# Performance work log

Measured on AMD Instinct MI355X. Metric: run time of the kernel, lower is better.

## Reference

```python
import jax, jax.numpy as jnp
import numpy as np

B, T, C, K, NH, HID, L, NC = 16, 500, 512, 7, 8, 2048, 3, 2
HD = C // NH
SCALE = float(1.0 / np.sqrt(HD))


def setup_inputs() -> dict:
    key = jax.random.key(0)
    ks = jax.random.split(key, 24)
    rn = lambda k, sh, s=0.02: jax.random.normal(k, sh, jnp.float32) * s
    return {
        'x': jax.random.normal(ks[0], (B, T, C), jnp.float32),
        'dw_w': rn(ks[1], (L, NC, C, 1, K)),   # depthwise conv kernels (groups=C)
        'dw_b': rn(ks[2], (L, NC, C)),
        'pw_w': rn(ks[3], (L, NC, C, C)),       # pointwise 1x1 conv weights [out,in]
        'pw_b': rn(ks[4], (L, NC, C)),
        'cln_g': jnp.ones((L, NC, C), jnp.float32),
        'cln_b': jnp.zeros((L, NC, C), jnp.float32),
        'wq': rn(ks[5], (L, C, C)), 'bq': rn(ks[6], (L, C)),
        'wk': rn(ks[7], (L, C, C)), 'bk': rn(ks[8], (L, C)),
        'wv': rn(ks[9], (L, C, C)), 'bv': rn(ks[10], (L, C)),
        'wo': rn(ks[11], (L, C, C)), 'bo': rn(ks[12], (L, C)),
        'aln_g': jnp.ones((L, C), jnp.float32), 'aln_b': jnp.zeros((L, C), jnp.float32),
        'w1': rn(ks[13], (L, HID, C)), 'b1': rn(ks[14], (L, HID)),
        'w2': rn(ks[15], (L, C, HID)), 'b2': rn(ks[16], (L, C)),
        'fln_g': jnp.ones((L, C), jnp.float32), 'fln_b': jnp.zeros((L, C), jnp.float32),
    }


def _ln(x, g, b):
    m = x.mean(-1, keepdims=True)
    v = ((x - m) ** 2).mean(-1, keepdims=True)
    return (x - m) / jnp.sqrt(v + 1e-5) * g + b


def _conv_block(x, w, b, pw, pb, g, be):
    # x: (B, C, T). Depthwise conv (groups=C), padding K//2 keeps T.
    out = jax.lax.conv_general_dilated(
        x, w, window_strides=(1,), padding=[(K // 2, K // 2)],
        feature_group_count=C, dimension_numbers=('NCH', 'OIH', 'NCH')) + b[None, :, None]
    out = jnp.einsum('bct,oc->bot', out, pw) + pb[None, :, None]  # pointwise 1x1
    out = _ln(out.transpose(0, 2, 1), g, be).transpose(0, 2, 1)
    return out


def _attn(x, wq, bq, wk, bk, wv, bv, wo, bo):
    Bx, Tx, Cx = x.shape
    def split(h):
        return h.reshape(Bx, Tx, NH, HD).transpose(0, 2, 1, 3)  # (B,H,T,HD)
    q = split(x @ wq.T + bq)
    k = split(x @ wk.T + bk)
    v = split(x @ wv.T + bv)
    att = jnp.einsum('bhqd,bhkd->bhqk', q, k) * SCALE
    mask = jnp.tril(jnp.ones((Tx, Tx), bool))
    att = jnp.where(mask, att, -1e10)
    att = jax.nn.softmax(att, axis=-1)
    y = jnp.einsum('bhqk,bhkd->bhqd', att, v)
    y = y.transpose(0, 2, 1, 3).reshape(Bx, Tx, Cx)
    return y @ wo.T + bo


def _block(x, l, dw_w, dw_b, pw_w, pw_b, cln_g, cln_b, wq, bq, wk, bk, wv, bv,
           wo, bo, aln_g, aln_b, w1, b1, w2, b2, fln_g, fln_b):
    out = x.transpose(0, 2, 1)  # (B, C, T)
    for c in range(NC):
        out = _conv_block(out, dw_w[l, c], dw_b[l, c], pw_w[l, c], pw_b[l, c],
                          cln_g[l, c], cln_b[l, c])
    out = out.transpose(0, 2, 1)  # (B, T, C)
    out = _attn(out, wq[l], bq[l], wk[l], bk[l], wv[l], bv[l], wo[l], bo[l])
    out = _ln(out, aln_g[l], aln_b[l])
    out = _ln(jax.nn.relu(out @ w1[l].T + b1[l]) @ w2[l].T + b2[l], fln_g[l], fln_b[l])
    return out  # eval mode: dropouts are identity


def reference(x, dw_w, dw_b, pw_w, pw_b, cln_g, cln_b, wq, bq, wk, bk, wv, bv,
              wo, bo, aln_g, aln_b, w1, b1, w2, b2, fln_g, fln_b):
    outs = []
    h = x
    for l in range(L):
        h = _block(h, l, dw_w, dw_b, pw_w, pw_b, cln_g, cln_b, wq, bq, wk, bk,
                   wv, bv, wo, bo, aln_g, aln_b, w1, b1, w2, b2, fln_g, fln_b)
        outs.append(h)
    return tuple(outs)
```

## Files before the change

### kernel.cpp

```cpp
#include <hip/hip_runtime.h>
#include <hip/hip_bf16.h>

namespace {
constexpr int B = 16, T = 500, C = 512, KW = 7, NH = 8, HD = 64, HID = 2048;
constexpr int M = B * T;
constexpr float SCALE = 0.125f;
constexpr int BTC = B * T * C;
constexpr int CC = C * C;
constexpr int SEG_PW0 = 0;
constexpr int SEG_PW1 = CC;
constexpr int SEG_WQ  = 2 * CC;
constexpr int SEG_WK  = 3 * CC;
constexpr int SEG_WV  = 4 * CC;
constexpr int SEG_WO  = 5 * CC;
constexpr int SEG_W1  = 6 * CC;
constexpr int SEG_W2  = 6 * CC + HID * C;
constexpr int SEG_END = 6 * CC + 2 * HID * C;
}

typedef short s16x8 __attribute__((ext_vector_type(8)));
typedef float f32x4v __attribute__((ext_vector_type(4)));
typedef unsigned short u16x4 __attribute__((ext_vector_type(4)));

__device__ __forceinline__ unsigned int bfrne(float f) {
  unsigned int u = __float_as_uint(f);
  return (u + 0x7fffu + ((u >> 16) & 1u)) >> 16;
}
__device__ __forceinline__ unsigned int pack2(float a, float b) {
  return bfrne(a) | (bfrne(b) << 16);
}

__device__ __forceinline__ void gl_lds16(const unsigned short* g,
                                         unsigned short* l) {
  __builtin_amdgcn_global_load_lds(
      (const __attribute__((address_space(1))) void*)g,
      (__attribute__((address_space(3))) void*)l, 16, 0, 0);
}

__global__ __launch_bounds__(256) void cvtw_kernel(
    const float* __restrict__ pw0, const float* __restrict__ pw1,
    const float* __restrict__ wqp, const float* __restrict__ wkp,
    const float* __restrict__ wvp, const float* __restrict__ wop,
    const float* __restrict__ w1p, const float* __restrict__ w2p,
    unsigned short* __restrict__ dst) {
  size_t e = ((size_t)blockIdx.x * 256 + threadIdx.x) * 8;
  const float* src;
  size_t off;
  if      (e < SEG_PW1) { src = pw0; off = e - SEG_PW0; }
  else if (e < SEG_WQ)  { src = pw1; off = e - SEG_PW1; }
  else if (e < SEG_WK)  { src = wqp; off = e - SEG_WQ; }
  else if (e < SEG_WV)  { src = wkp; off = e - SEG_WK; }
  else if (e < SEG_WO)  { src = wvp; off = e - SEG_WV; }
  else if (e < SEG_W1)  { src = wop; off = e - SEG_WO; }
  else if (e < SEG_W2)  { src = w1p; off = e - SEG_W1; }
  else                  { src = w2p; off = e - SEG_W2; }
  float4 a = *(const float4*)(src + off);
  float4 b = *(const float4*)(src + off + 4);
  uint4 o;
  o.x = pack2(a.x, a.y); o.y = pack2(a.z, a.w);
  o.z = pack2(b.x, b.y); o.w = pack2(b.z, b.w);
  *(uint4*)(dst + e) = o;
}

__global__ __launch_bounds__(256) void biascat_kernel(
    const float* __restrict__ bq, const float* __restrict__ bk,
    const float* __restrict__ bv, float* __restrict__ dst) {
  int i = blockIdx.x * 256 + threadIdx.x;
  float v = (i < 512) ? bq[i] : (i < 1024 ? bk[i - 512] : bv[i - 1024]);
  dst[i] = v;
}

template <bool RELU, bool YBF, bool SPLIT>
__global__ __launch_bounds__(512) void gemm_mfma(
    const unsigned short* __restrict__ Xb,
    const unsigned short* __restrict__ Wb, const float* __restrict__ bias,
    void* __restrict__ Yv, int N, int K) {
  __shared__ unsigned short As[3][128 * 32];
  __shared__ unsigned short Bs[3][128 * 32];
  const int tid = threadIdx.x;
  const int w = tid >> 6, lane = tid & 63;
  const int quad = lane >> 4, r15 = lane & 15;

  const int ks = SPLIT ? blockIdx.z : 0;
  const int K2 = SPLIT ? (K >> 1) : K;
  const int kbase = ks * K2;

  const int gx = gridDim.x;
  const int nwg = gx * gridDim.y;
  const int orig = blockIdx.y * gx + blockIdx.x;
  const int q8 = nwg >> 3, r8 = nwg & 7;
  const int xcd = orig & 7, sidx = orig >> 3;
  const int tile =
      (xcd < r8 ? xcd * (q8 + 1) : r8 * (q8 + 1) + (xcd - r8) * q8) + sidx;
  const int n0 = (tile % gx) * 128;
  const int m0 = (tile / gx) * 128;

  const int srow = lane >> 2;
  const int gch = ((lane & 3) ^ ((lane >> 3) & 3)) * 8;
  const size_t xsrc =
      (size_t)min(m0 + w * 16 + srow, M - 1) * K + kbase + gch;
  const size_t wsrc = (size_t)(n0 + w * 16 + srow) * K + kbase + gch;

  auto issue = [&](int buf, int k0) {
    gl_lds16(Xb + xsrc + k0, &As[buf][w * 512]);
    gl_lds16(Wb + wsrc + k0, &Bs[buf][w * 512]);
  };

  const int wm = w >> 1, wn = w & 1;
  const int mh = wm * 32, nh = wn * 64;
  const int c0 = (quad ^ ((r15 >> 1) & 3)) * 8;

  f32x4v acc[2][4];
#pragma unroll
  for (int i = 0; i < 2; ++i)
#pragma unroll
    for (int j = 0; j < 4; ++j) acc[i][j] = {0.f, 0.f, 0.f, 0.f};

  const int nk = K2 / 32;
  issue(0, 0);
  issue(1, 32);
  int cur = 0, nxt = 2;
  for (int c = 0; c < nk; ++c) {
    if (c + 1 < nk)
      asm volatile("s_waitcnt vmcnt(2)" ::: "memory");
    else
      asm volatile("s_waitcnt vmcnt(0)" ::: "memory");
    __builtin_amdgcn_s_barrier();
    __builtin_amdgcn_sched_barrier(0);
    if (c + 2 < nk) issue(nxt, (c + 2) * 32);
    const unsigned short* Ac = As[cur];
    const unsigned short* Bc = Bs[cur];
    s16x8 af[2], bg[4];
#pragma unroll
    for (int im = 0; im < 2; ++im)
      af[im] = *(const s16x8*)&Ac[(mh + im * 16 + r15) * 32 + c0];
#pragma unroll
    for (int in = 0; in < 4; ++in)
      bg[in] = *(const s16x8*)&Bc[(nh + in * 16 + r15) * 32 + c0];
#pragma unroll
    for (int in = 0; in < 4; ++in)
#pragma unroll
      for (int im = 0; im < 2; ++im)
        acc[im][in] = __builtin_amdgcn_mfma_f32_16x16x32_bf16(
            af[im], bg[in], acc[im][in], 0, 0, 0);
    cur = (cur == 2) ? 0 : cur + 1;
    nxt = (nxt == 2) ? 0 : nxt + 1;
  }
  float* Yf = (float*)Yv + (SPLIT ? (size_t)ks * M * N : 0);
#pragma unroll
  for (int in = 0; in < 4; ++in) {
    int col = n0 + nh + in * 16 + r15;
    float bv = bias[col];
    if (SPLIT && ks) bv = 0.f;
#pragma unroll
    for (int im = 0; im < 2; ++im) {
      int rowb = m0 + mh + im * 16 + quad * 4;
#pragma unroll
      for (int r = 0; r < 4; ++r) {
        int row = rowb + r;
        if (row < M) {
          float v = acc[im][in][r] + bv;
          if (RELU) v = fmaxf(v, 0.f);
          if (YBF)
            ((unsigned short*)Yv)[(size_t)row * N + col] =
                (unsigned short)bfrne(v);
          else
            Yf[(size_t)row * N + col] = v;
        }
      }
    }
  }
}

__global__ __launch_bounds__(256) void dwconv_kernel(
    const float* __restrict__ X, const float* __restrict__ W,
    const float* __restrict__ bias, unsigned short* __restrict__ Y) {
  int gid = blockIdx.x * 256 + threadIdx.x;
  int b = blockIdx.y;
  int e = gid * 2;
  int t = e >> 9;
  int c = e & 511;
  float acc0 = bias[c], acc1 = bias[c + 1];
  size_t base = (size_t)b * T * C;
#pragma unroll
  for (int k = 0; k < KW; ++k) {
    int tt = t + k - 3;
    if (tt >= 0 && tt < T) {
      float2 xv = *(const float2*)&X[base + (size_t)tt * C + c];
      acc0 += xv.x * W[c * KW + k];
      acc1 += xv.y * W[(c + 1) * KW + k];
    }
  }
  *(unsigned int*)&Y[base + e] = pack2(acc0, acc1);
}

template <bool DUAL, bool SUM2>
__global__ __launch_bounds__(256) void ln_kernel(
    const float* __restrict__ X, const float* __restrict__ g,
    const float* __restrict__ bta, float* __restrict__ Y,
    unsigned short* __restrict__ Yb) {
  int row = blockIdx.x * 4 + (threadIdx.x >> 6);
  int lane = threadIdx.x & 63;
  const float* x = X + (size_t)row * C + lane * 8;
  float4 a = *(const float4*)x;
  float4 b2 = *(const float4*)(x + 4);
  float v[8] = {a.x, a.y, a.z, a.w, b2.x, b2.y, b2.z, b2.w};
  if (SUM2) {
    const float* x2 = x + (size_t)BTC;
    float4 a2 = *(const float4*)x2;
    float4 b3 = *(const float4*)(x2 + 4);
    v[0] += a2.x; v[1] += a2.y; v[2] += a2.z; v[3] += a2.w;
    v[4] += b3.x; v[5] += b3.y; v[6] += b3.z; v[7] += b3.w;
  }
  float s = 0.f, ss = 0.f;
#pragma unroll
  for (int i = 0; i < 8; ++i) {
    s += v[i];
    ss += v[i] * v[i];
  }
#pragma unroll
  for (int off = 32; off; off >>= 1) {
    s += __shfl_xor(s, off);
    ss += __shfl_xor(ss, off);
  }
  float mean = s * (1.f / C);
  float var = ss * (1.f / C) - mean * mean;
  var = fmaxf(var, 0.f);
  float rstd = rsqrtf(var + 1e-5f);
  float4 g0 = *(const float4*)(g + lane * 8);
  float4 g1 = *(const float4*)(g + lane * 8 + 4);
  float4 be0 = *(const float4*)(bta + lane * 8);
  float4 be1 = *(const float4*)(bta + lane * 8 + 4);
  float gg[8] = {g0.x, g0.y, g0.z, g0.w, g1.x, g1.y, g1.z, g1.w};
  float bb[8] = {be0.x, be0.y, be0.z, be0.w, be1.x, be1.y, be1.z, be1.w};
  float o[8];
#pragma unroll
  for (int i = 0; i < 8; ++i) o[i] = (v[i] - mean) * rstd * gg[i] + bb[i];
  float* y = Y + (size_t)row * C + lane * 8;
  float4 w0 = {o[0], o[1], o[2], o[3]};
  float4 w1 = {o[4], o[5], o[6], o[7]};
  *(float4*)y = w0;
  *(float4*)(y + 4) = w1;
  if (DUAL) {
    uint4 ob;
    ob.x = pack2(o[0], o[1]); ob.y = pack2(o[2], o[3]);
    ob.z = pack2(o[4], o[5]); ob.w = pack2(o[6], o[7]);
    *(uint4*)(Yb + (size_t)row * C + lane * 8) = ob;
  }
}

__global__ __launch_bounds__(256) void attn_mfma_kernel(
    const unsigned short* __restrict__ QKV, unsigned short* __restrict__ Yb) {
  constexpr int QS = 3 * C;
  constexpr int LDK = 72;
  __shared__ __align__(16) unsigned short Ks[64 * LDK];
  __shared__ __align__(16) unsigned short Vt[64 * LDK];
  __shared__ __align__(16) unsigned short Ps[4][16 * LDK];
  const int tid = threadIdx.x;
  const int lane = tid & 63, w = tid >> 6;
  const int quad = lane >> 4, r15 = lane & 15;
  const int qt = blockIdx.x, hh = blockIdx.y, b = blockIdx.z;
  const int q0 = qt * 64;
  const size_t hbase = (size_t)hh * HD;

  s16x8 qa[2];
  {
    int qr = min(q0 + w * 16 + r15, T - 1);
    const unsigned short* qp = QKV + ((size_t)b * T + qr) * QS + hbase;
#pragma unroll
    for (int ks = 0; ks < 2; ++ks)
      qa[ks] = *(const s16x8*)(qp + ks * 32 + quad * 8);
  }

  f32x4v oacc[4];
  float mm[4], ll[4];
#pragma unroll
  for (int i = 0; i < 4; ++i) {
    oacc[i] = {0.f, 0.f, 0.f, 0.f};
    mm[i] = -1e30f;
    ll[i] = 0.f;
  }

  const int krow = tid >> 2, kd = (tid & 3) * 16;
  const int vk4 = (tid >> 4) * 4, vd4 = (tid & 15) * 4;

  const int kend = min(q0 + 63, T - 1);
  for (int key0 = 0; key0 <= kend; key0 += 64) {
    __syncthreads();
    {
      int key = key0 + krow;
      if (key < T) {
        const unsigned short* kp =
            QKV + ((size_t)b * T + key) * QS + C + hbase + kd;
        uint4 k0 = *(const uint4*)kp;
        uint4 k1 = *(const uint4*)(kp + 8);
        *(uint4*)&Ks[krow * LDK + kd] = k0;
        *(uint4*)&Ks[krow * LDK + kd + 8] = k1;
      } else {
        uint4 z = {0u, 0u, 0u, 0u};
        *(uint4*)&Ks[krow * LDK + kd] = z;
        *(uint4*)&Ks[krow * LDK + kd + 8] = z;
      }
    }
    {
      u16x4 va[4];
#pragma unroll
      for (int j = 0; j < 4; ++j) {
        int key = key0 + vk4 + j;
        if (key < T) {
          va[j] = *(const u16x4*)(QKV + ((size_t)b * T + key) * QS + 2 * C +
                                  hbase + vd4);
        } else {
          va[j] = (u16x4){0, 0, 0, 0};
        }
      }
#pragma unroll
      for (int i = 0; i < 4; ++i) {
        uint2 o2;
        o2.x = (unsigned int)va[0][i] | ((unsigned int)va[1][i] << 16);
        o2.y = (unsigned int)va[2][i] | ((unsigned int)va[3][i] << 16);
        *(uint2*)&Vt[(vd4 + i) * LDK + vk4] = o2;
      }
    }
    __syncthreads();

    f32x4v sa[4];
#pragma unroll
    for (int nt = 0; nt < 4; ++nt) {
      s16x8 kb0 = *(const s16x8*)&Ks[(nt * 16 + r15) * LDK + quad * 8];
      s16x8 kb1 = *(const s16x8*)&Ks[(nt * 16 + r15) * LDK + 32 + quad * 8];
      f32x4v z = {0.f, 0.f, 0.f, 0.f};
      z = __builtin_amdgcn_mfma_f32_16x16x32_bf16(qa[0], kb0, z, 0, 0, 0);
      z = __builtin_amdgcn_mfma_f32_16x16x32_bf16(qa[1], kb1, z, 0, 0, 0);
      sa[nt] = z;
    }
    const bool diag = (key0 == q0);

#pragma unroll
    for (int r = 0; r < 4; ++r) {
      int q = q0 + w * 16 + quad * 4 + r;
      float sv[4];
#pragma unroll
      for (int nt = 0; nt < 4; ++nt) {
        sv[nt] = sa[nt][r] * SCALE;
        if (diag && (key0 + nt * 16 + r15 > q)) sv[nt] = -1e30f;
      }
      float mx = fmaxf(fmaxf(sv[0], sv[1]), fmaxf(sv[2], sv[3]));
      mx = fmaxf(mx, __shfl_xor(mx, 8));
      mx = fmaxf(mx, __shfl_xor(mx, 4));
      mx = fmaxf(mx, __shfl_xor(mx, 2));
      mx = fmaxf(mx, __shfl_xor(mx, 1));
      float mnew = fmaxf(mm[r], mx);
      float alpha = __expf(mm[r] - mnew);
      float ps = 0.f;
#pragma unroll
      for (int nt = 0; nt < 4; ++nt) {
        float p = __expf(sv[nt] - mnew);
        ps += p;
        Ps[w][(quad * 4 + r) * LDK + nt * 16 + r15] =
            (unsigned short)bfrne(p);
      }
      ps += __shfl_xor(ps, 8);
      ps += __shfl_xor(ps, 4);
      ps += __shfl_xor(ps, 2);
      ps += __shfl_xor(ps, 1);
      ll[r] = ll[r] * alpha + ps;
      mm[r] = mnew;
#pragma unroll
      for (int dt = 0; dt < 4; ++dt) oacc[dt][r] *= alpha;
    }
    asm volatile("s_waitcnt lgkmcnt(0)" ::: "memory");
    __builtin_amdgcn_sched_barrier(0);

    s16x8 pa0 = *(const s16x8*)&Ps[w][r15 * LDK + quad * 8];
    s16x8 pa1 = *(const s16x8*)&Ps[w][r15 * LDK + 32 + quad * 8];
#pragma unroll
    for (int dt = 0; dt < 4; ++dt) {
      s16x8 vb0 = *(const s16x8*)&Vt[(dt * 16 + r15) * LDK + quad * 8];
      s16x8 vb1 = *(const s16x8*)&Vt[(dt * 16 + r15) * LDK + 32 + quad * 8];
      oacc[dt] =
          __builtin_amdgcn_mfma_f32_16x16x32_bf16(pa0, vb0, oacc[dt], 0, 0, 0);
      oacc[dt] =
          __builtin_amdgcn_mfma_f32_16x16x32_bf16(pa1, vb1, oacc[dt], 0, 0, 0);
    }
  }

#pragma unroll
  for (int r = 0; r < 4; ++r) {
    int q = q0 + w * 16 + quad * 4 + r;
    if (q < T) {
      float inv = 1.f / ll[r];
      unsigned short* yp = Yb + ((size_t)b * T + q) * C + hbase;
#pragma unroll
      for (int dt = 0; dt < 4; ++dt)
        yp[dt * 16 + r15] = (unsigned short)bfrne(oacc[dt][r] * inv);
    }
  }
}

extern "C" void kernel_launch(void* const* d_in, const int* in_sizes, int n_in,
                              void* d_out, int out_size, void* d_ws,
                              size_t ws_size, hipStream_t stream) {
  const float* x     = (const float*)d_in[0];
  const float* dw_w  = (const float*)d_in[1];
  const float* dw_b  = (const float*)d_in[2];
  const float* pw_w  = (const float*)d_in[3];
  const float* pw_b  = (const float*)d_in[4];
  const float* cln_g = (const float*)d_in[5];
  const float* cln_b = (const float*)d_in[6];
  const float* wq    = (const float*)d_in[7];
  const float* bq    = (const float*)d_in[8];
  const float* wk    = (const float*)d_in[9];
  const float* bk    = (const float*)d_in[10];
  const float* wv    = (const float*)d_in[11];
  const float* bv    = (const float*)d_in[12];
  const float* wo    = (const float*)d_in[13];
  const float* bo    = (const float*)d_in[14];
  const float* aln_g = (const float*)d_in[15];
  const float* aln_b = (const float*)d_in[16];
  const float* w1    = (const float*)d_in[17];
  const float* b1    = (const float*)d_in[18];
  const float* w2    = (const float*)d_in[19];
  const float* b2    = (const float*)d_in[20];
  const float* fln_g = (const float*)d_in[21];
  const float* fln_b = (const float*)d_in[22];

  float* ws = (float*)d_ws;
  float* A  = ws;
  float* Bf = ws + (size_t)BTC;
  float* R0 = ws + (size_t)2 * BTC;
  float* R1 = ws + (size_t)3 * BTC;
  float* R2 = ws + (size_t)4 * BTC;
  unsigned short* WA = (unsigned short*)(ws + (size_t)5 * BTC);
  float* out = (float*)d_out;

  unsigned short* xbf   = (unsigned short*)Bf;
  unsigned short* qkvbf = (unsigned short*)R0;
  unsigned short* fbf   = (unsigned short*)R2;
  unsigned short* hbf   = (unsigned short*)A;
  float* qkvb = A;

  dim3 blk(256);
  dim3 blkG(512);
  dim3 gemmC2(C / 128, 63, 2);
  dim3 gemmQKV(3 * C / 128, 63);
  dim3 gemmH(HID / 128, 63);
  dim3 convG(T * C / 512, B);
  dim3 attnG((T + 63) / 64, NH, B);
  int cvtwB = SEG_END / 2048;

  for (int l = 0; l < 3; ++l) {
    float* h = out + (size_t)l * BTC;
    const float* hin = (l == 0) ? x : out + (size_t)(l - 1) * BTC;
    cvtw_kernel<<<cvtwB, blk, 0, stream>>>(
        pw_w + (size_t)(2 * l) * CC, pw_w + (size_t)(2 * l + 1) * CC,
        wq + (size_t)l * CC, wk + (size_t)l * CC, wv + (size_t)l * CC,
        wo + (size_t)l * CC, w1 + (size_t)l * HID * C,
        w2 + (size_t)l * C * HID, WA);
    biascat_kernel<<<6, blk, 0, stream>>>(bq + (size_t)l * C,
                                          bk + (size_t)l * C,
                                          bv + (size_t)l * C, qkvb);
    for (int cb = 0; cb < 2; ++cb) {
      int lc = l * 2 + cb;
      const float* src = (cb == 0) ? hin : h;
      dwconv_kernel<<<convG, blk, 0, stream>>>(src, dw_w + (size_t)lc * C * KW,
                                               dw_b + (size_t)lc * C, xbf);
      gemm_mfma<false, false, true><<<gemmC2, blkG, 0, stream>>>(
          xbf, WA + (cb ? SEG_PW1 : SEG_PW0), pw_b + (size_t)lc * C, R0, C, C);
      if (cb == 0)
        ln_kernel<false, true><<<M / 4, blk, 0, stream>>>(
            R0, cln_g + (size_t)lc * C, cln_b + (size_t)lc * C, h, nullptr);
      else
        ln_kernel<true, true><<<M / 4, blk, 0, stream>>>(
            R0, cln_g + (size_t)lc * C, cln_b + (size_t)lc * C, h, xbf);
    }
    gemm_mfma<false, true, false><<<gemmQKV, blkG, 0, stream>>>(
        xbf, WA + SEG_WQ, qkvb, qkvbf, 3 * C, C);
    attn_mfma_kernel<<<attnG, blk, 0, stream>>>(qkvbf, xbf);
    gemm_mfma<false, false, true><<<gemmC2, blkG, 0, stream>>>(
        xbf, WA + SEG_WO, bo + (size_t)l * C, R0, C, C);
    ln_kernel<true, true><<<M / 4, blk, 0, stream>>>(
        R0, aln_g + (size_t)l * C, aln_b + (size_t)l * C, h, fbf);
    gemm_mfma<true, true, false><<<gemmH, blkG, 0, stream>>>(
        fbf, WA + SEG_W1, b1 + (size_t)l * HID, hbf, HID, C);
    gemm_mfma<false, false, true><<<gemmC2, blkG, 0, stream>>>(
        hbf, WA + SEG_W2, b2 + (size_t)l * C, R0, C, HID);
    ln_kernel<false, true><<<M / 4, blk, 0, stream>>>(
        R0, fln_g + (size_t)l * C, fln_b + (size_t)l * C, h, nullptr);
  }
}
```

Before: 977.6 us.

## Restructure causal attention: 128-query blocks, register-prefetched K/V, swizzled V tile

The attention kernel now uses 512-thread blocks covering 128 queries, so each K/V tile loaded into shared memory is reused by twice as many waves. The next K/V tile is prefetched into registers while the current tile is computed, and the V transpose layout is XOR-swizzled to reduce LDS bank conflicts. Blocks are launched in reverse order so the longest causal tiles start first, waves skip fully masked tiles, and MFMA sections get raised priority. The risks are fewer blocks in the grid, higher register pressure, and idle waves at the diagonal tiles.

```diff
diff --git a/kernel.cpp b/kernel.cpp
--- a/kernel.cpp
+++ b/kernel.cpp
@@ -249,27 +249,28 @@
   }
 }
 
-__global__ __launch_bounds__(256) void attn_mfma_kernel(
+__global__ __launch_bounds__(512) void attn_mfma_kernel(
     const unsigned short* __restrict__ QKV, unsigned short* __restrict__ Yb) {
   constexpr int QS = 3 * C;
   constexpr int LDK = 72;
   __shared__ __align__(16) unsigned short Ks[64 * LDK];
   __shared__ __align__(16) unsigned short Vt[64 * LDK];
-  __shared__ __align__(16) unsigned short Ps[4][16 * LDK];
+  __shared__ __align__(16) unsigned short Ps[8][16 * LDK];
   const int tid = threadIdx.x;
   const int lane = tid & 63, w = tid >> 6;
   const int quad = lane >> 4, r15 = lane & 15;
-  const int qt = blockIdx.x, hh = blockIdx.y, b = blockIdx.z;
-  const int q0 = qt * 64;
+  const int qt = (gridDim.x - 1) - blockIdx.x;
+  const int hh = blockIdx.y, b = blockIdx.z;
+  const int q0 = qt * 128;
   const size_t hbase = (size_t)hh * HD;
+  const size_t bT = (size_t)b * T;
 
   s16x8 qa[2];
   {
     int qr = min(q0 + w * 16 + r15, T - 1);
-    const unsigned short* qp = QKV + ((size_t)b * T + qr) * QS + hbase;
-#pragma unroll
-    for (int ks = 0; ks < 2; ++ks)
-      qa[ks] = *(const s16x8*)(qp + ks * 32 + quad * 8);
+    const unsigned short* qp = QKV + (bT + qr) * QS + hbase;
+    qa[0] = *(const s16x8*)(qp + quad * 8);
+    qa[1] = *(const s16x8*)(qp + 32 + quad * 8);
   }
 
   f32x4v oacc[4];
@@ -281,107 +282,130 @@
     ll[i] = 0.f;
   }
 
-  const int krow = tid >> 2, kd = (tid & 3) * 16;
-  const int vk4 = (tid >> 4) * 4, vd4 = (tid & 15) * 4;
-
-  const int kend = min(q0 + 63, T - 1);
+  const int krow = tid >> 3, kd = (tid & 7) * 8;
+  const int vd4 = (tid & 15) * 4;
+  const int vk2 = (tid >> 4) * 2;
+  const int vsub = vk2 & 7;
+  const int vkc = vk2 >> 3;
+  const int pc8 = (vkc ^ (tid & 7)) * 8;
+
+  auto loadK = [&](int key0, uint4& kreg) {
+    int key = key0 + krow;
+    if (key < T)
+      kreg = *(const uint4*)(QKV + (bT + key) * QS + C + hbase + kd);
+    else
+      kreg = (uint4){0u, 0u, 0u, 0u};
+  };
+  auto loadV = [&](int key0, u16x4* vreg) {
+#pragma unroll
+    for (int j = 0; j < 2; ++j) {
+      int key = key0 + vk2 + j;
+      if (key < T)
+        vreg[j] = *(const u16x4*)(QKV + (bT + key) * QS + 2 * C + hbase + vd4);
+      else
+        vreg[j] = (u16x4){0, 0, 0, 0};
+    }
+  };
+  auto storeKV = [&](uint4 kreg, const u16x4* vreg) {
+    *(uint4*)&Ks[krow * LDK + kd] = kreg;
+#pragma unroll
+    for (int i = 0; i < 4; ++i) {
+      unsigned int o = (unsigned int)(unsigned short)vreg[0][i] |
+                       ((unsigned int)(unsigned short)vreg[1][i] << 16);
+      *(unsigned int*)&Vt[(vd4 + i) * LDK + pc8 + vsub] = o;
+    }
+  };
+
+  const int kend = min(q0 + 127, T - 1);
+  const int myqmax = q0 + w * 16 + 15;
+
+  uint4 kr;
+  u16x4 vr[2];
+  loadK(0, kr);
+  loadV(0, vr);
   for (int key0 = 0; key0 <= kend; key0 += 64) {
     __syncthreads();
-    {
-      int key = key0 + krow;
-      if (key < T) {
-        const unsigned short* kp =
-            QKV + ((size_t)b * T + key) * QS + C + hbase + kd;
-        uint4 k0 = *(const uint4*)kp;
-        uint4 k1 = *(const uint4*)(kp + 8);
-        *(uint4*)&Ks[krow * LDK + kd] = k0;
-        *(uint4*)&Ks[krow * LDK + kd + 8] = k1;
-      } else {
-        uint4 z = {0u, 0u, 0u, 0u};
-        *(uint4*)&Ks[krow * LDK + kd] = z;
-        *(uint4*)&Ks[krow * LDK + kd + 8] = z;
+    storeKV(kr, vr);
+    const bool more = (key0 + 64 <= kend);
+    uint4 nk;
+    u16x4 nv[2];
+    if (more) {
+      loadK(key0 + 64, nk);
+      loadV(key0 + 64, nv);
+    }
+    __syncthreads();
+    if (key0 <= myqmax) {
+      f32x4v sa[4];
+      __builtin_amdgcn_s_setprio(1);
+#pragma unroll
+      for (int nt = 0; nt < 4; ++nt) {
+        s16x8 kb0 = *(const s16x8*)&Ks[(nt * 16 + r15) * LDK + quad * 8];
+        s16x8 kb1 = *(const s16x8*)&Ks[(nt * 16 + r15) * LDK + 32 + quad * 8];
+        f32x4v z = {0.f, 0.f, 0.f, 0.f};
+        z = __builtin_amdgcn_mfma_f32_16x16x32_bf16(qa[0], kb0, z, 0, 0, 0);
+        z = __builtin_amdgcn_mfma_f32_16x16x32_bf16(qa[1], kb1, z, 0, 0, 0);
+        sa[nt] = z;
       }
-    }
-    {
-      u16x4 va[4];
-#pragma unroll
-      for (int j = 0; j < 4; ++j) {
-        int key = key0 + vk4 + j;
-        if (key < T) {
-          va[j] = *(const u16x4*)(QKV + ((size_t)b * T + key) * QS + 2 * C +
-                                  hbase + vd4);
-        } else {
-          va[j] = (u16x4){0, 0, 0, 0};
+      __builtin_amdgcn_s_setprio(0);
+      const bool needmask = (key0 + 63 > q0 + w * 16);
+
+#pragma unroll
+      for (int r = 0; r < 4; ++r) {
+        int q = q0 + w * 16 + quad * 4 + r;
+        if (q >= T) continue;
+        float sv[4];
+#pragma unroll
+        for (int nt = 0; nt < 4; ++nt) {
+          sv[nt] = sa[nt][r] * SCALE;
+          if (needmask && (key0 + nt * 16 + r15 > q)) sv[nt] = -1e30f;
         }
+        float mx = fmaxf(fmaxf(sv[0], sv[1]), fmaxf(sv[2], sv[3]));
+        mx = fmaxf(mx, __shfl_xor(mx, 8));
+        mx = fmaxf(mx, __shfl_xor(mx, 4));
+        mx = fmaxf(mx, __shfl_xor(mx, 2));
+        mx = fmaxf(mx, __shfl_xor(mx, 1));
+        float mnew = fmaxf(mm[r], mx);
+        float alpha = __expf(mm[r] - mnew);
+        float ps = 0.f;
+#pragma unroll
+        for (int nt = 0; nt < 4; ++nt) {
+          float p = __expf(sv[nt] - mnew);
+          ps += p;
+          Ps[w][(quad * 4 + r) * LDK + nt * 16 + r15] =
+              (unsigned short)bfrne(p);
+        }
+        ps += __shfl_xor(ps, 8);
+        ps += __shfl_xor(ps, 4);
+        ps += __shfl_xor(ps, 2);
+        ps += __shfl_xor(ps, 1);
+        ll[r] = ll[r] * alpha + ps;
+        mm[r] = mnew;
+#pragma unroll
+        for (int dt = 0; dt < 4; ++dt) oacc[dt][r] *= alpha;
       }
-#pragma unroll
-      for (int i = 0; i < 4; ++i) {
-        uint2 o2;
-        o2.x = (unsigned int)va[0][i] | ((unsigned int)va[1][i] << 16);
-        o2.y = (unsigned int)va[2][i] | ((unsigned int)va[3][i] << 16);
-        *(uint2*)&Vt[(vd4 + i) * LDK + vk4] = o2;
+      asm volatile("s_waitcnt lgkmcnt(0)" ::: "memory");
+      __builtin_amdgcn_sched_barrier(0);
+
+      s16x8 pa0 = *(const s16x8*)&Ps[w][r15 * LDK + quad * 8];
+      s16x8 pa1 = *(const s16x8*)&Ps[w][r15 * LDK + 32 + quad * 8];
+      __builtin_amdgcn_s_setprio(1);
+#pragma unroll
+      for (int dt = 0; dt < 4; ++dt) {
+        const int rd = dt * 16 + r15;
+        const int fr = (rd >> 2) & 7;
+        s16x8 vb0 = *(const s16x8*)&Vt[rd * LDK + (quad ^ fr) * 8];
+        s16x8 vb1 = *(const s16x8*)&Vt[rd * LDK + ((quad + 4) ^ fr) * 8];
+        oacc[dt] = __builtin_amdgcn_mfma_f32_16x16x32_bf16(pa0, vb0,
+                                                           oacc[dt], 0, 0, 0);
+        oacc[dt] = __builtin_amdgcn_mfma_f32_16x16x32_bf16(pa1, vb1,
+                                                           oacc[dt], 0, 0, 0);
       }
-    }
-    __syncthreads();
-
-    f32x4v sa[4];
-#pragma unroll
-    for (int nt = 0; nt < 4; ++nt) {
-      s16x8 kb0 = *(const s16x8*)&Ks[(nt * 16 + r15) * LDK + quad * 8];
-      s16x8 kb1 = *(const s16x8*)&Ks[(nt * 16 + r15) * LDK + 32 + quad * 8];
-      f32x4v z = {0.f, 0.f, 0.f, 0.f};
-      z = __builtin_amdgcn_mfma_f32_16x16x32_bf16(qa[0], kb0, z, 0, 0, 0);
-      z = __builtin_amdgcn_mfma_f32_16x16x32_bf16(qa[1], kb1, z, 0, 0, 0);
-      sa[nt] = z;
-    }
-    const bool diag = (key0 == q0);
-
-#pragma unroll
-    for (int r = 0; r < 4; ++r) {
-      int q = q0 + w * 16 + quad * 4 + r;
-      float sv[4];
-#pragma unroll
-      for (int nt = 0; nt < 4; ++nt) {
-        sv[nt] = sa[nt][r] * SCALE;
-        if (diag && (key0 + nt * 16 + r15 > q)) sv[nt] = -1e30f;
-      }
-      float mx = fmaxf(fmaxf(sv[0], sv[1]), fmaxf(sv[2], sv[3]));
-      mx = fmaxf(mx, __shfl_xor(mx, 8));
-      mx = fmaxf(mx, __shfl_xor(mx, 4));
-      mx = fmaxf(mx, __shfl_xor(mx, 2));
-      mx = fmaxf(mx, __shfl_xor(mx, 1));
-      float mnew = fmaxf(mm[r], mx);
-      float alpha = __expf(mm[r] - mnew);
-      float ps = 0.f;
-#pragma unroll
-      for (int nt = 0; nt < 4; ++nt) {
-        float p = __expf(sv[nt] - mnew);
-        ps += p;
-        Ps[w][(quad * 4 + r) * LDK + nt * 16 + r15] =
-            (unsigned short)bfrne(p);
-      }
-      ps += __shfl_xor(ps, 8);
-      ps += __shfl_xor(ps, 4);
-      ps += __shfl_xor(ps, 2);
-      ps += __shfl_xor(ps, 1);
-      ll[r] = ll[r] * alpha + ps;
-      mm[r] = mnew;
-#pragma unroll
-      for (int dt = 0; dt < 4; ++dt) oacc[dt][r] *= alpha;
-    }
-    asm volatile("s_waitcnt lgkmcnt(0)" ::: "memory");
-    __builtin_amdgcn_sched_barrier(0);
-
-    s16x8 pa0 = *(const s16x8*)&Ps[w][r15 * LDK + quad * 8];
-    s16x8 pa1 = *(const s16x8*)&Ps[w][r15 * LDK + 32 + quad * 8];
-#pragma unroll
-    for (int dt = 0; dt < 4; ++dt) {
-      s16x8 vb0 = *(const s16x8*)&Vt[(dt * 16 + r15) * LDK + quad * 8];
-      s16x8 vb1 = *(const s16x8*)&Vt[(dt * 16 + r15) * LDK + 32 + quad * 8];
-      oacc[dt] =
-          __builtin_amdgcn_mfma_f32_16x16x32_bf16(pa0, vb0, oacc[dt], 0, 0, 0);
-      oacc[dt] =
-          __builtin_amdgcn_mfma_f32_16x16x32_bf16(pa1, vb1, oacc[dt], 0, 0, 0);
+      __builtin_amdgcn_s_setprio(0);
+    }
+    if (more) {
+      kr = nk;
+      vr[0] = nv[0];
+      vr[1] = nv[1];
     }
   }
 
@@ -390,7 +414,7 @@
     int q = q0 + w * 16 + quad * 4 + r;
     if (q < T) {
       float inv = 1.f / ll[r];
-      unsigned short* yp = Yb + ((size_t)b * T + q) * C + hbase;
+      unsigned short* yp = Yb + (bT + q) * C + hbase;
 #pragma unroll
       for (int dt = 0; dt < 4; ++dt)
         yp[dt * 16 + r15] = (unsigned short)bfrne(oacc[dt][r] * inv);
@@ -446,7 +470,7 @@
   dim3 gemmQKV(3 * C / 128, 63);
   dim3 gemmH(HID / 128, 63);
   dim3 convG(T * C / 512, B);
-  dim3 attnG((T + 63) / 64, NH, B);
+  dim3 attnG((T + 127) / 128, NH, B);
   int cvtwB = SEG_END / 2048;
 
   for (int l = 0; l < 3; ++l) {
@@ -476,7 +500,7 @@
     }
     gemm_mfma<false, true, false><<<gemmQKV, blkG, 0, stream>>>(
         xbf, WA + SEG_WQ, qkvb, qkvbf, 3 * C, C);
-    attn_mfma_kernel<<<attnG, blk, 0, stream>>>(qkvbf, xbf);
+    attn_mfma_kernel<<<attnG, blkG, 0, stream>>>(qkvbf, xbf);
     gemm_mfma<false, false, true><<<gemmC2, blkG, 0, stream>>>(
         xbf, WA + SEG_WO, bo + (size_t)l * C, R0, C, C);
     ln_kernel<true, true><<<M / 4, blk, 0, stream>>>(
```

Result: no change. 974.2 us (-0.3%).
